# Kernel optimization log

Measured on AMD Instinct MI355X. Metric: run time of the kernel, lower is better.

The kernel has to match this reference:

```python
import jax, jax.numpy as jnp
import numpy as np

NUM_EMBEDDINGS = 8192
EMBEDDING_DIM = 256
BETA = 0.25


def setup_inputs() -> dict:
    key = jax.random.key(0)
    k1, k2 = jax.random.split(key)
    z = jax.random.normal(k1, (2, EMBEDDING_DIM, 4, 32, 32), dtype=jnp.float32)
    # nn.init.uniform_(embedding.weight, -1/ne, 1/ne)
    emb_weight = jax.random.uniform(
        k2, (NUM_EMBEDDINGS, EMBEDDING_DIM), dtype=jnp.float32,
        minval=-1.0 / NUM_EMBEDDINGS, maxval=1.0 / NUM_EMBEDDINGS)
    return {"z": z, "emb_weight": emb_weight}


def reference(z, emb_weight):
    # channel_last: [N, D, T, H, W] -> [N, T, H, W, D]
    z_l = jnp.moveaxis(z, 1, -1)
    # squared distance (up to a constant ||z||^2 which does not affect argmin)
    # d[..., e] = ||w_e||^2 - 2 <z, w_e>
    d = jnp.sum(emb_weight ** 2, axis=1) - 2.0 * jnp.einsum(
        '...d,ed->...e', z_l, emb_weight)
    index = jnp.argmin(d, axis=-1)                      # [N, T, H, W]
    z_q = emb_weight[index]                             # [N, T, H, W, D]
    loss = (jnp.mean((jax.lax.stop_gradient(z_q) - z_l) ** 2)
            + BETA * jnp.mean((z_q - jax.lax.stop_gradient(z_l)) ** 2))
    # straight-through estimator
    z_q = z_l + jax.lax.stop_gradient(z_q - z_l)
    # channel_first: [N, T, H, W, D] -> [N, D, T, H, W]
    z_q = jnp.moveaxis(z_q, -1, 1)
    return z_q, loss, index
```

## Files before the change

kernel.cpp:

```cpp
#include <hip/hip_runtime.h>
#include <cstdint>
#include <cstddef>

#define NE      8192
#define DIM     256
#define NPOS    8192
#define ZELEMS  2097152
#define NSTRIDE 1048576
#define SPATIAL 4096

#define KTOT    576
#define KSTEP   64
#define NSTEPS  9
#define ROWB    1152
#define ES      8
#define PBLK    256

typedef _Float16 half8 __attribute__((ext_vector_type(8)));
typedef float    f32x4 __attribute__((ext_vector_type(4)));

__device__ __forceinline__ unsigned ordmap(float f) {
    unsigned u = __float_as_uint(f);
    return u ^ (unsigned)(((int)u >> 31) | 0x80000000);
}
__device__ __forceinline__ float unord(unsigned long long k) {
    unsigned v = (unsigned)(k >> 13);
    unsigned u = (v & 0x80000000u) ? (v ^ 0x80000000u) : ~v;
    return __uint_as_float(u);
}

__global__ void conv_z(const float* __restrict__ z, _Float16* __restrict__ Apk) {
    __shared__ float zt[256 * 64];
    const int tid = threadIdx.x;
    const int pbase = blockIdx.x * 64;
    const int n = pbase >> 12;
    const int sbase = pbase & (SPATIAL - 1);
    const float* zsrc = z + (size_t)n * NSTRIDE + sbase;
    for (int i = tid; i < 256 * 64; i += 256) {
        int d = i >> 6, p = i & 63;
        zt[i] = zsrc[(size_t)d * SPATIAL + p];
    }
    __syncthreads();
    const int p = tid & 63, seg = tid >> 6;
    _Float16* rowp = Apk + (size_t)(pbase + p) * KTOT;
    for (int j8 = 0; j8 < 8; ++j8) {
        half8 hv, lv;
        #pragma unroll
        for (int jj = 0; jj < 8; ++jj) {
            int d = seg * 64 + j8 * 8 + jj;
            float v = -2.0f * zt[d * 64 + p];
            _Float16 h = (_Float16)v;
            hv[jj] = h;
            lv[jj] = (_Float16)(v - (float)h);
        }
        *(half8*)(rowp + seg * 64 + j8 * 8) = hv;
        *(half8*)(rowp + 256 + seg * 64 + j8 * 8) = lv;
    }
    if (tid < 64) {
        _Float16* r2 = Apk + (size_t)(pbase + tid) * KTOT + 512;
        #pragma unroll
        for (int q = 0; q < 8; ++q) {
            half8 v8;
            #pragma unroll
            for (int jj = 0; jj < 8; ++jj) v8[jj] = (_Float16)0.0f;
            if (q == 0) { v8[0] = (_Float16)1.0f; v8[1] = (_Float16)1.0f; }
            *(half8*)(r2 + q * 8) = v8;
        }
    }
}

__global__ void conv_w(const float* __restrict__ w, _Float16* __restrict__ Bpk) {
    __shared__ float red[4];
    const int e = blockIdx.x, t = threadIdx.x;
    float v = w[(size_t)e * DIM + t];
    float vs = v * 8192.0f;
    _Float16 h = (_Float16)vs;
    _Float16 l = (_Float16)(vs - (float)h);
    _Float16* row = Bpk + (size_t)e * KTOT;
    row[t] = h;
    row[256 + t] = l;
    float sq = v * v;
    #pragma unroll
    for (int off = 32; off; off >>= 1) sq += __shfl_down(sq, off);
    if ((t & 63) == 0) red[t >> 6] = sq;
    __syncthreads();
    if (t == 0) {
        float nrm = 8192.0f * (red[0] + red[1] + red[2] + red[3]);
        _Float16 nh = (_Float16)nrm;
        row[512] = nh;
        row[513] = (_Float16)(nrm - (float)nh);
    }
    if (t >= 2 && t < 64) row[512 + t] = (_Float16)0.0f;
}

__global__ __launch_bounds__(512, 2) void vq_gemm(
        const _Float16* __restrict__ Apk, const _Float16* __restrict__ Bpk,
        unsigned long long* __restrict__ parts) {
    __shared__ _Float16 Asl[2][PBLK * KSTEP];
    __shared__ _Float16 Bsl[2][256 * KSTEP];

    const int tid = threadIdx.x;
    const int lane = tid & 63;
    const int wid = tid >> 6;
    const int wm = wid >> 2, wn = wid & 3;
    const int es = blockIdx.x & 7, pt = blockIdx.x >> 3;
    const int l15 = lane & 15, l4 = lane >> 4, l7 = lane & 7;
    const int co0 = (l4 ^ l7) << 4;
    const int co1 = ((4 + l4) ^ l7) << 4;
    const int aoff = (wm * 128 + l15) * 128;
    const int boff = (wn * 64 + l15) * 128;

    const int srow = tid >> 3;
    const int schunk = tid & 7;
    const int sw = ((schunk ^ (srow & 7)) << 4);

    const char* Ag = (const char*)(Apk + (size_t)pt * PBLK * KTOT);
    const char* Bg0 = (const char*)(Bpk + (size_t)es * 1024 * KTOT);

    const int AKT[NSTEPS] = {0,1,2,3, 4,5,6,7, 8};
    const int BKT[NSTEPS] = {0,1,2,3, 0,1,2,3, 8};

#define STAGE(gbase, lbase, ktv) {                                          \
        _Pragma("unroll")                                                   \
        for (int i_ = 0; i_ < 4; ++i_) {                                    \
            int r_ = srow + i_ * 64;                                        \
            const char* g_ = (gbase) + (size_t)r_ * ROWB + (ktv) * 128 + sw;\
            char* lp_ = (char*)(lbase) + r_ * 128 + schunk * 16;            \
            __builtin_amdgcn_global_load_lds(                               \
                (const __attribute__((address_space(1))) void*)g_,          \
                (__attribute__((address_space(3))) void*)lp_, 16, 0, 0);    \
        } }

    float b1[4], b2[4]; int e1[4];
    #pragma unroll
    for (int q = 0; q < 4; ++q) { b1[q] = 3.0e38f; b2[q] = 3.0e38f; e1[q] = 0; }

    for (int st = 0; st < 4; ++st) {
        const char* Bg = Bg0 + (size_t)st * 256 * ROWB;
        STAGE(Ag, Asl[0], 0);
        STAGE(Bg, Bsl[0], 0);
        __syncthreads();

        f32x4 acc[8][4];
        #pragma unroll
        for (int mi = 0; mi < 8; ++mi)
            #pragma unroll
            for (int ni = 0; ni < 4; ++ni) acc[mi][ni] = (f32x4)0.0f;

        #pragma unroll
        for (int kt = 0; kt < NSTEPS; ++kt) {
            const int cb = kt & 1;
            if (kt < NSTEPS - 1) {
                STAGE(Ag, Asl[cb ^ 1], AKT[kt + 1]);
                STAGE(Bg, Bsl[cb ^ 1], BKT[kt + 1]);
            }
            const char* Ab = (const char*)Asl[cb];
            const char* Bb = (const char*)Bsl[cb];
            #pragma unroll
            for (int kb = 0; kb < 2; ++kb) {
                const int co = kb ? co1 : co0;
                half8 af[8], bf[4];
                #pragma unroll
                for (int mi = 0; mi < 8; ++mi)
                    af[mi] = *(const half8*)(Bb + aoff + mi * 2048 + co);
                #pragma unroll
                for (int ni = 0; ni < 4; ++ni)
                    bf[ni] = *(const half8*)(Ab + boff + ni * 2048 + co);
                #pragma unroll
                for (int mi = 0; mi < 8; ++mi)
                    #pragma unroll
                    for (int ni = 0; ni < 4; ++ni)
                        acc[mi][ni] = __builtin_amdgcn_mfma_f32_16x16x32_f16(
                            af[mi], bf[ni], acc[mi][ni], 0, 0, 0);
            }
            __syncthreads();
        }

        const int ebl = es * 1024 + st * 256 + wm * 128 + (l4 << 2);
        #pragma unroll
        for (int mi = 0; mi < 8; ++mi)
            #pragma unroll
            for (int ni = 0; ni < 4; ++ni)
                #pragma unroll
                for (int r = 0; r < 4; ++r) {
                    float v = acc[mi][ni][r];
                    int e = ebl + mi * 16 + r;
                    bool c = v < b1[ni];
                    b2[ni] = fminf(b2[ni], fmaxf(v, b1[ni]));
                    b1[ni] = c ? v : b1[ni];
                    e1[ni] = c ? e : e1[ni];
                }
    }

    #pragma unroll
    for (int ni = 0; ni < 4; ++ni) {
        unsigned long long k1 =
            (((unsigned long long)ordmap(b1[ni])) << 13) | (unsigned)e1[ni];
        unsigned long long k2 = ((unsigned long long)ordmap(b2[ni])) << 13;
        #pragma unroll
        for (int m = 16; m <= 32; m <<= 1) {
            unsigned long long o1 = __shfl_xor(k1, m, 64);
            unsigned long long o2 = __shfl_xor(k2, m, 64);
            unsigned long long mx = k1 > o1 ? k1 : o1;
            k1 = k1 < o1 ? k1 : o1;
            k2 = k2 < o2 ? k2 : o2;
            k2 = k2 < mx ? k2 : mx;
        }
        if (lane < 16) {
            int pos = pt * PBLK + wn * 64 + ni * 16 + l15;
            unsigned long long* pp = parts + (((size_t)(wm * 8 + es)) * NPOS + pos) * 2;
            pp[0] = k1; pp[1] = k2;
        }
    }
#undef STAGE
}

__global__ void vq_combine(const unsigned long long* __restrict__ parts,
                           unsigned long long* __restrict__ keys,
                           int* __restrict__ count, int* __restrict__ list) {
    int pos = blockIdx.x * 256 + threadIdx.x;
    unsigned long long g1 = ~0ull, g2 = ~0ull;
    for (int s = 0; s < 16; ++s) {
        const unsigned long long* pp = parts + (((size_t)s) * NPOS + pos) * 2;
        unsigned long long a1 = pp[0], a2 = pp[1];
        unsigned long long mx = g1 > a1 ? g1 : a1;
        g1 = g1 < a1 ? g1 : a1;
        g2 = g2 < a2 ? g2 : a2;
        g2 = g2 < mx ? g2 : mx;
    }
    if (unord(g2) - unord(g1) < 0.05f) {
        int ix = atomicAdd(count, 1);
        list[ix] = pos;
        keys[pos] = ~0ull;
    } else {
        keys[pos] = g1;
    }
}

#define NCHUNK 32
__global__ void vq_exact(const float* __restrict__ z, const float* __restrict__ w,
                         const int* __restrict__ list, const int* __restrict__ count,
                         unsigned long long* __restrict__ keys) {
    __shared__ float zv[256];
    __shared__ unsigned long long wk[4];
    const int t = threadIdx.x;
    int cnt = *count; if (cnt > NPOS) cnt = NPOS;
    int nwork = cnt * NCHUNK;
    for (int item = blockIdx.x; item < nwork; item += gridDim.x) {
        int pos = list[item >> 5];
        int c = item & (NCHUNK - 1);
        int n = pos >> 12, s = pos & (SPATIAL - 1);
        zv[t] = z[(size_t)n * NSTRIDE + (size_t)t * SPATIAL + s];
        __syncthreads();

        int e = c * 256 + t;
        const float* wr = w + (size_t)e * DIM;
        double nrm = 0.0, dt = 0.0;
        #pragma unroll 4
        for (int d = 0; d < DIM; d += 4) {
            float4 w4 = *(const float4*)(wr + d);
            nrm += (double)w4.x * w4.x + (double)w4.y * w4.y
                 + (double)w4.z * w4.z + (double)w4.w * w4.w;
            dt  += (double)w4.x * zv[d] + (double)w4.y * zv[d + 1]
                 + (double)w4.z * zv[d + 2] + (double)w4.w * zv[d + 3];
        }
        float sc = (float)(8192.0 * (nrm - 2.0 * dt));
        unsigned long long k = (((unsigned long long)ordmap(sc)) << 13) | (unsigned)e;
        #pragma unroll
        for (int off = 32; off; off >>= 1) {
            unsigned long long o = __shfl_down(k, off, 64);
            k = k < o ? k : o;
        }
        if ((t & 63) == 0) wk[t >> 6] = k;
        __syncthreads();
        if (t == 0) {
            unsigned long long m0 = wk[0] < wk[1] ? wk[0] : wk[1];
            unsigned long long m1 = wk[2] < wk[3] ? wk[2] : wk[3];
            unsigned long long m = m0 < m1 ? m0 : m1;
            atomicMin(&keys[pos], m);
        }
        __syncthreads();
    }
}

__global__ void vq_out(const float* __restrict__ z, const float* __restrict__ w,
                       const unsigned long long* __restrict__ keys,
                       float* __restrict__ out, float* __restrict__ partial) {
    __shared__ float red[4];
    int gi = blockIdx.x * 256 + threadIdx.x;
    int n = gi >> 20;
    int r = gi & (NSTRIDE - 1);
    int d = r >> 12;
    int s = r & (SPATIAL - 1);
    int p = (n << 12) | s;

    int e = (int)(keys[p] & 8191ull);
    float zl = z[gi];
    float zq = w[(size_t)e * DIM + d];
    out[gi] = zl + (zq - zl);

    float diff = zq - zl;
    float ls = diff * diff;
    #pragma unroll
    for (int off = 32; off; off >>= 1) ls += __shfl_down(ls, off);
    if ((threadIdx.x & 63) == 0) red[threadIdx.x >> 6] = ls;
    __syncthreads();
    if (threadIdx.x == 0) partial[blockIdx.x] = red[0] + red[1] + red[2] + red[3];

    if (gi < NPOS) {
        int ei = (int)(keys[gi] & 8191ull);
        out[ZELEMS + 1 + gi] = (float)ei;
    }
}

__global__ void vq_loss_final(const float* __restrict__ partial, float* __restrict__ out) {
    __shared__ float red[4];
    float sum = 0.f;
    for (int i = threadIdx.x; i < 8192; i += 256) sum += partial[i];
    #pragma unroll
    for (int off = 32; off; off >>= 1) sum += __shfl_down(sum, off);
    if ((threadIdx.x & 63) == 0) red[threadIdx.x >> 6] = sum;
    __syncthreads();
    if (threadIdx.x == 0)
        out[ZELEMS] = 1.25f * (red[0] + red[1] + red[2] + red[3]) / (float)ZELEMS;
}

extern "C" void kernel_launch(void* const* d_in, const int* in_sizes, int n_in,
                              void* d_out, int out_size, void* d_ws, size_t ws_size,
                              hipStream_t stream) {
    const float* z = (const float*)d_in[0];
    const float* w = (const float*)d_in[1];
    float* out = (float*)d_out;

    char* wsb = (char*)d_ws;
    _Float16* Apk = (_Float16*)(wsb);
    _Float16* Bpk = (_Float16*)(wsb + 9437184);
    unsigned long long* parts = (unsigned long long*)(wsb + 18874368);
    unsigned long long* keys  = (unsigned long long*)(wsb + 20971520);
    int*   count   = (int*)(wsb + 21037056);
    int*   list    = (int*)(wsb + 21037072);
    float* partial = (float*)(wsb + 21069856);

    hipMemsetAsync(count, 0, 4, stream);

    conv_z <<<NPOS / 64, 256, 0, stream>>>(z, Apk);
    conv_w <<<NE, 256, 0, stream>>>(w, Bpk);
    vq_gemm<<<(NPOS / PBLK) * ES, 512, 0, stream>>>(Apk, Bpk, parts);
    vq_combine<<<NPOS / 256, 256, 0, stream>>>(parts, keys, count, list);
    vq_exact<<<1024, 256, 0, stream>>>(z, w, list, count, keys);
    vq_out <<<ZELEMS / 256, 256, 0, stream>>>(z, w, keys, out, partial);
    vq_loss_final<<<1, 256, 0, stream>>>(partial, out);
}
```

Before: 307.9 us.

## Fuse conversion kernels, interleave GEMM staging with MFMA phases, fold loss reduction

Merges the z and codebook fp16 conversion kernels into one launch. The codebook part now handles four rows per block with vectorised loads and a wave-level norm reduction. The GEMM inner loop is split into four MFMA phases, with async LDS staging spread across them and s_barrier/setprio added so memory and matrix work overlap. The final loss reduction moves into vq_out using a last-block atomic counter, which removes the memset and one launch but adds extra barriers and an atomic per block.

```diff
diff --git a/kernel.cpp b/kernel.cpp
--- a/kernel.cpp
+++ b/kernel.cpp
@@ -17,6 +17,7 @@
 #define PBLK    256
 
 typedef _Float16 half8 __attribute__((ext_vector_type(8)));
+typedef _Float16 half4 __attribute__((ext_vector_type(4)));
 typedef float    f32x4 __attribute__((ext_vector_type(4)));
 
 __device__ __forceinline__ unsigned ordmap(float f) {
@@ -29,68 +30,73 @@
     return __uint_as_float(u);
 }
 
-__global__ void conv_z(const float* __restrict__ z, _Float16* __restrict__ Apk) {
-    __shared__ float zt[256 * 64];
+__global__ void conv_fused(const float* __restrict__ z, const float* __restrict__ w,
+                           _Float16* __restrict__ Apk, _Float16* __restrict__ Bpk,
+                           int* __restrict__ count, int* __restrict__ done) {
     const int tid = threadIdx.x;
-    const int pbase = blockIdx.x * 64;
-    const int n = pbase >> 12;
-    const int sbase = pbase & (SPATIAL - 1);
-    const float* zsrc = z + (size_t)n * NSTRIDE + sbase;
-    for (int i = tid; i < 256 * 64; i += 256) {
-        int d = i >> 6, p = i & 63;
-        zt[i] = zsrc[(size_t)d * SPATIAL + p];
-    }
-    __syncthreads();
-    const int p = tid & 63, seg = tid >> 6;
-    _Float16* rowp = Apk + (size_t)(pbase + p) * KTOT;
-    for (int j8 = 0; j8 < 8; ++j8) {
-        half8 hv, lv;
-        #pragma unroll
-        for (int jj = 0; jj < 8; ++jj) {
-            int d = seg * 64 + j8 * 8 + jj;
-            float v = -2.0f * zt[d * 64 + p];
-            _Float16 h = (_Float16)v;
-            hv[jj] = h;
-            lv[jj] = (_Float16)(v - (float)h);
-        }
-        *(half8*)(rowp + seg * 64 + j8 * 8) = hv;
-        *(half8*)(rowp + 256 + seg * 64 + j8 * 8) = lv;
-    }
-    if (tid < 64) {
-        _Float16* r2 = Apk + (size_t)(pbase + tid) * KTOT + 512;
-        #pragma unroll
-        for (int q = 0; q < 8; ++q) {
-            half8 v8;
-            #pragma unroll
-            for (int jj = 0; jj < 8; ++jj) v8[jj] = (_Float16)0.0f;
-            if (q == 0) { v8[0] = (_Float16)1.0f; v8[1] = (_Float16)1.0f; }
-            *(half8*)(r2 + q * 8) = v8;
-        }
-    }
-}
-
-__global__ void conv_w(const float* __restrict__ w, _Float16* __restrict__ Bpk) {
-    __shared__ float red[4];
-    const int e = blockIdx.x, t = threadIdx.x;
-    float v = w[(size_t)e * DIM + t];
-    float vs = v * 8192.0f;
-    _Float16 h = (_Float16)vs;
-    _Float16 l = (_Float16)(vs - (float)h);
-    _Float16* row = Bpk + (size_t)e * KTOT;
-    row[t] = h;
-    row[256 + t] = l;
-    float sq = v * v;
-    #pragma unroll
-    for (int off = 32; off; off >>= 1) sq += __shfl_down(sq, off);
-    if ((t & 63) == 0) red[t >> 6] = sq;
-    __syncthreads();
-    if (t == 0) {
-        float nrm = 8192.0f * (red[0] + red[1] + red[2] + red[3]);
+    if (blockIdx.x == 0 && tid == 0) { *count = 0; *done = 0; }
+
+    if (blockIdx.x < 128) {
+        __shared__ float zt[256 * 64];
+        const int pbase = blockIdx.x * 64;
+        const int n = pbase >> 12;
+        const int sbase = pbase & (SPATIAL - 1);
+        const float* zsrc = z + (size_t)n * NSTRIDE + sbase;
+        for (int i = tid; i < 256 * 64; i += 256) {
+            int d = i >> 6, p = i & 63;
+            zt[i] = zsrc[(size_t)d * SPATIAL + p];
+        }
+        __syncthreads();
+        const int p = tid & 63, seg = tid >> 6;
+        _Float16* rowp = Apk + (size_t)(pbase + p) * KTOT;
+        for (int j8 = 0; j8 < 8; ++j8) {
+            half8 hv, lv;
+            #pragma unroll
+            for (int jj = 0; jj < 8; ++jj) {
+                int d = seg * 64 + j8 * 8 + jj;
+                float v = -2.0f * zt[d * 64 + p];
+                _Float16 h = (_Float16)v;
+                hv[jj] = h;
+                lv[jj] = (_Float16)(v - (float)h);
+            }
+            *(half8*)(rowp + seg * 64 + j8 * 8) = hv;
+            *(half8*)(rowp + 256 + seg * 64 + j8 * 8) = lv;
+        }
+        if (tid < 64) {
+            _Float16* r2 = Apk + (size_t)(pbase + tid) * KTOT + 512;
+            #pragma unroll
+            for (int q = 0; q < 8; ++q) {
+                half8 v8;
+                #pragma unroll
+                for (int jj = 0; jj < 8; ++jj) v8[jj] = (_Float16)0.0f;
+                if (q == 0) { v8[0] = (_Float16)1.0f; v8[1] = (_Float16)1.0f; }
+                *(half8*)(r2 + q * 8) = v8;
+            }
+        }
+    } else {
+        const int lane = tid & 63;
+        const int e = (blockIdx.x - 128) * 4 + (tid >> 6);
+        const float4 v = *(const float4*)(w + (size_t)e * DIM + lane * 4);
+        half4 h, l;
+        {
+            float a0 = v.x * 8192.0f, a1 = v.y * 8192.0f,
+                  a2 = v.z * 8192.0f, a3 = v.w * 8192.0f;
+            h[0] = (_Float16)a0; l[0] = (_Float16)(a0 - (float)h[0]);
+            h[1] = (_Float16)a1; l[1] = (_Float16)(a1 - (float)h[1]);
+            h[2] = (_Float16)a2; l[2] = (_Float16)(a2 - (float)h[2]);
+            h[3] = (_Float16)a3; l[3] = (_Float16)(a3 - (float)h[3]);
+        }
+        _Float16* row = Bpk + (size_t)e * KTOT;
+        *(half4*)(row + lane * 4) = h;
+        *(half4*)(row + 256 + lane * 4) = l;
+        float sq = v.x * v.x + v.y * v.y + v.z * v.z + v.w * v.w;
+        #pragma unroll
+        for (int off = 32; off; off >>= 1) sq += __shfl_down(sq, off);
+        float nrm = __shfl(sq, 0) * 8192.0f;
         _Float16 nh = (_Float16)nrm;
-        row[512] = nh;
-        row[513] = (_Float16)(nrm - (float)nh);
-    }
-    if (t >= 2 && t < 64) row[512 + t] = (_Float16)0.0f;
+        _Float16 nl = (_Float16)(nrm - (float)nh);
+        row[512 + lane] = (lane == 0) ? nh : (lane == 1) ? nl : (_Float16)0.0f;
+    }
 }
 
 __global__ __launch_bounds__(512, 2) void vq_gemm(
@@ -120,9 +126,9 @@
     const int AKT[NSTEPS] = {0,1,2,3, 4,5,6,7, 8};
     const int BKT[NSTEPS] = {0,1,2,3, 0,1,2,3, 8};
 
-#define STAGE(gbase, lbase, ktv) {                                          \
+#define STAGE_R(gbase, lbase, ktv, IBEG, IEND) {                            \
         _Pragma("unroll")                                                   \
-        for (int i_ = 0; i_ < 4; ++i_) {                                    \
+        for (int i_ = (IBEG); i_ < (IEND); ++i_) {                          \
             int r_ = srow + i_ * 64;                                        \
             const char* g_ = (gbase) + (size_t)r_ * ROWB + (ktv) * 128 + sw;\
             char* lp_ = (char*)(lbase) + r_ * 128 + schunk * 16;            \
@@ -137,8 +143,8 @@
 
     for (int st = 0; st < 4; ++st) {
         const char* Bg = Bg0 + (size_t)st * 256 * ROWB;
-        STAGE(Ag, Asl[0], 0);
-        STAGE(Bg, Bsl[0], 0);
+        STAGE_R(Ag, Asl[0], AKT[0], 0, 4);
+        STAGE_R(Bg, Bsl[0], BKT[0], 0, 4);
         __syncthreads();
 
         f32x4 acc[8][4];
@@ -150,29 +156,66 @@
         #pragma unroll
         for (int kt = 0; kt < NSTEPS; ++kt) {
             const int cb = kt & 1;
-            if (kt < NSTEPS - 1) {
-                STAGE(Ag, Asl[cb ^ 1], AKT[kt + 1]);
-                STAGE(Bg, Bsl[cb ^ 1], BKT[kt + 1]);
-            }
             const char* Ab = (const char*)Asl[cb];
             const char* Bb = (const char*)Bsl[cb];
-            #pragma unroll
-            for (int kb = 0; kb < 2; ++kb) {
-                const int co = kb ? co1 : co0;
-                half8 af[8], bf[4];
-                #pragma unroll
-                for (int mi = 0; mi < 8; ++mi)
-                    af[mi] = *(const half8*)(Bb + aoff + mi * 2048 + co);
-                #pragma unroll
-                for (int ni = 0; ni < 4; ++ni)
-                    bf[ni] = *(const half8*)(Ab + boff + ni * 2048 + co);
-                #pragma unroll
-                for (int mi = 0; mi < 8; ++mi)
-                    #pragma unroll
-                    for (int ni = 0; ni < 4; ++ni)
-                        acc[mi][ni] = __builtin_amdgcn_mfma_f32_16x16x32_f16(
-                            af[mi], bf[ni], acc[mi][ni], 0, 0, 0);
-            }
+            const bool hn = (kt < NSTEPS - 1);
+            half8 af0[8], af1[8], bfp[2];
+
+            #pragma unroll
+            for (int mi = 0; mi < 8; ++mi)
+                af0[mi] = *(const half8*)(Bb + aoff + mi * 2048 + co0);
+            bfp[0] = *(const half8*)(Ab + boff + 0 * 2048 + co0);
+            bfp[1] = *(const half8*)(Ab + boff + 1 * 2048 + co0);
+            if (hn) STAGE_R(Ag, Asl[cb ^ 1], AKT[kt + 1], 0, 4);
+            __builtin_amdgcn_s_barrier();
+            __builtin_amdgcn_s_setprio(1);
+            #pragma unroll
+            for (int mi = 0; mi < 8; ++mi) {
+                acc[mi][0] = __builtin_amdgcn_mfma_f32_16x16x32_f16(af0[mi], bfp[0], acc[mi][0], 0, 0, 0);
+                acc[mi][1] = __builtin_amdgcn_mfma_f32_16x16x32_f16(af0[mi], bfp[1], acc[mi][1], 0, 0, 0);
+            }
+            __builtin_amdgcn_s_setprio(0);
+            __builtin_amdgcn_s_barrier();
+
+            bfp[0] = *(const half8*)(Ab + boff + 2 * 2048 + co0);
+            bfp[1] = *(const half8*)(Ab + boff + 3 * 2048 + co0);
+            if (hn) STAGE_R(Bg, Bsl[cb ^ 1], BKT[kt + 1], 0, 2);
+            __builtin_amdgcn_s_barrier();
+            __builtin_amdgcn_s_setprio(1);
+            #pragma unroll
+            for (int mi = 0; mi < 8; ++mi) {
+                acc[mi][2] = __builtin_amdgcn_mfma_f32_16x16x32_f16(af0[mi], bfp[0], acc[mi][2], 0, 0, 0);
+                acc[mi][3] = __builtin_amdgcn_mfma_f32_16x16x32_f16(af0[mi], bfp[1], acc[mi][3], 0, 0, 0);
+            }
+            __builtin_amdgcn_s_setprio(0);
+            __builtin_amdgcn_s_barrier();
+
+            #pragma unroll
+            for (int mi = 0; mi < 8; ++mi)
+                af1[mi] = *(const half8*)(Bb + aoff + mi * 2048 + co1);
+            bfp[0] = *(const half8*)(Ab + boff + 0 * 2048 + co1);
+            bfp[1] = *(const half8*)(Ab + boff + 1 * 2048 + co1);
+            if (hn) STAGE_R(Bg, Bsl[cb ^ 1], BKT[kt + 1], 2, 4);
+            __builtin_amdgcn_s_barrier();
+            __builtin_amdgcn_s_setprio(1);
+            #pragma unroll
+            for (int mi = 0; mi < 8; ++mi) {
+                acc[mi][0] = __builtin_amdgcn_mfma_f32_16x16x32_f16(af1[mi], bfp[0], acc[mi][0], 0, 0, 0);
+                acc[mi][1] = __builtin_amdgcn_mfma_f32_16x16x32_f16(af1[mi], bfp[1], acc[mi][1], 0, 0, 0);
+            }
+            __builtin_amdgcn_s_setprio(0);
+            __builtin_amdgcn_s_barrier();
+
+            bfp[0] = *(const half8*)(Ab + boff + 2 * 2048 + co1);
+            bfp[1] = *(const half8*)(Ab + boff + 3 * 2048 + co1);
+            __builtin_amdgcn_s_barrier();
+            __builtin_amdgcn_s_setprio(1);
+            #pragma unroll
+            for (int mi = 0; mi < 8; ++mi) {
+                acc[mi][2] = __builtin_amdgcn_mfma_f32_16x16x32_f16(af1[mi], bfp[0], acc[mi][2], 0, 0, 0);
+                acc[mi][3] = __builtin_amdgcn_mfma_f32_16x16x32_f16(af1[mi], bfp[1], acc[mi][3], 0, 0, 0);
+            }
+            __builtin_amdgcn_s_setprio(0);
             __syncthreads();
         }
 
@@ -212,7 +255,7 @@
             pp[0] = k1; pp[1] = k2;
         }
     }
-#undef STAGE
+#undef STAGE_R
 }
 
 __global__ void vq_combine(const unsigned long long* __restrict__ parts,
@@ -285,9 +328,12 @@
 
 __global__ void vq_out(const float* __restrict__ z, const float* __restrict__ w,
                        const unsigned long long* __restrict__ keys,
-                       float* __restrict__ out, float* __restrict__ partial) {
+                       float* __restrict__ out, float* __restrict__ partial,
+                       int* __restrict__ done) {
     __shared__ float red[4];
-    int gi = blockIdx.x * 256 + threadIdx.x;
+    __shared__ int isLast;
+    const int tid = threadIdx.x;
+    int gi = blockIdx.x * 256 + tid;
     int n = gi >> 20;
     int r = gi & (NSTRIDE - 1);
     int d = r >> 12;
@@ -303,26 +349,30 @@
     float ls = diff * diff;
     #pragma unroll
     for (int off = 32; off; off >>= 1) ls += __shfl_down(ls, off);
-    if ((threadIdx.x & 63) == 0) red[threadIdx.x >> 6] = ls;
-    __syncthreads();
-    if (threadIdx.x == 0) partial[blockIdx.x] = red[0] + red[1] + red[2] + red[3];
+    if ((tid & 63) == 0) red[tid >> 6] = ls;
 
     if (gi < NPOS) {
         int ei = (int)(keys[gi] & 8191ull);
         out[ZELEMS + 1 + gi] = (float)ei;
     }
-}
-
-__global__ void vq_loss_final(const float* __restrict__ partial, float* __restrict__ out) {
-    __shared__ float red[4];
-    float sum = 0.f;
-    for (int i = threadIdx.x; i < 8192; i += 256) sum += partial[i];
-    #pragma unroll
-    for (int off = 32; off; off >>= 1) sum += __shfl_down(sum, off);
-    if ((threadIdx.x & 63) == 0) red[threadIdx.x >> 6] = sum;
     __syncthreads();
-    if (threadIdx.x == 0)
-        out[ZELEMS] = 1.25f * (red[0] + red[1] + red[2] + red[3]) / (float)ZELEMS;
+    if (tid == 0) {
+        partial[blockIdx.x] = red[0] + red[1] + red[2] + red[3];
+        __threadfence();
+        isLast = (atomicAdd(done, 1) == (int)gridDim.x - 1);
+    }
+    __syncthreads();
+    if (isLast) {
+        __threadfence();
+        float sum = 0.f;
+        for (int i = tid; i < 8192; i += 256) sum += partial[i];
+        #pragma unroll
+        for (int off = 32; off; off >>= 1) sum += __shfl_down(sum, off);
+        if ((tid & 63) == 0) red[tid >> 6] = sum;
+        __syncthreads();
+        if (tid == 0)
+            out[ZELEMS] = 1.25f * (red[0] + red[1] + red[2] + red[3]) / (float)ZELEMS;
+    }
 }
 
 extern "C" void kernel_launch(void* const* d_in, const int* in_sizes, int n_in,
@@ -338,16 +388,13 @@
     unsigned long long* parts = (unsigned long long*)(wsb + 18874368);
     unsigned long long* keys  = (unsigned long long*)(wsb + 20971520);
     int*   count   = (int*)(wsb + 21037056);
+    int*   done    = (int*)(wsb + 21037060);
     int*   list    = (int*)(wsb + 21037072);
     float* partial = (float*)(wsb + 21069856);
 
-    hipMemsetAsync(count, 0, 4, stream);
-
-    conv_z <<<NPOS / 64, 256, 0, stream>>>(z, Apk);
-    conv_w <<<NE, 256, 0, stream>>>(w, Bpk);
+    conv_fused<<<128 + NE / 4, 256, 0, stream>>>(z, w, Apk, Bpk, count, done);
     vq_gemm<<<(NPOS / PBLK) * ES, 512, 0, stream>>>(Apk, Bpk, parts);
     vq_combine<<<NPOS / 256, 256, 0, stream>>>(parts, keys, count, list);
     vq_exact<<<1024, 256, 0, stream>>>(z, w, list, count, keys);
-    vq_out <<<ZELEMS / 256, 256, 0, stream>>>(z, w, keys, out, partial);
-    vq_loss_final<<<1, 256, 0, stream>>>(partial, out);
-}
+    vq_out<<<ZELEMS / 256, 256, 0, stream>>>(z, w, keys, out, partial, done);
+}
```

Result: slower. 479.1 us (+55.6%).
